# Kernel tuning notes

Measured on AMD Instinct MI355X. Metric: run time of the kernel, lower is better.

## Reference

```python
import jax, jax.numpy as jnp
import numpy as np

HIER_WEIGHT = 0.1

def setup_inputs() -> dict:
    key = jax.random.key(0)
    k1, k2, k3, k4, k5 = jax.random.split(key, 5)
    B, N, D = 128, 100000, 256
    E = N - 1
    return {
        "logits": jax.random.normal(k1, (B, N), dtype=jnp.float32),
        "labels": jax.random.randint(k2, (B,), 0, N, dtype=jnp.int64),
        "label_emb": jax.random.normal(k3, (N, D), dtype=jnp.float32),
        "parent_idx": jax.random.randint(k4, (E,), 0, N, dtype=jnp.int64),
        "child_idx": jax.random.randint(k5, (E,), 0, N, dtype=jnp.int64),
    }

def reference(logits, labels, label_emb, parent_idx, child_idx):
    # base loss: mean cross-entropy over the batch (loss_fn)
    logp = jax.nn.log_softmax(logits, axis=-1)                      # [B, N]
    ce = -jnp.take_along_axis(logp, labels[:, None], axis=-1)       # [B, 1]
    base_loss = jnp.mean(ce)
    # hierarchy penalty: sum over all (parent, child) edges of ||p - c||_2^2
    diff = label_emb[parent_idx] - label_emb[child_idx]             # [E, D]
    recursive_loss = jnp.sum(diff * diff)
    return base_loss + HIER_WEIGHT * recursive_loss
```

## Files before the change

### kernel.cpp

```cpp
#include <hip/hip_runtime.h>
#include <math.h>


#define CE_SLICES   8
#define CE_THREADS  256
#define EDGE_BATCH  32
#define EDGE_THREADS 256

__global__ __launch_bounds__(CE_THREADS) void ce_partial_kernel(
    const float* __restrict__ logits, float* __restrict__ ws_ce, int N)
{
    const int row   = blockIdx.x >> 3;
    const int slice = blockIdx.x & (CE_SLICES - 1);
    const int n4    = N >> 2;
    const int per   = n4 / CE_SLICES;
    const float4* __restrict__ rp4 =
        (const float4*)(logits + (size_t)row * (size_t)N) + (size_t)slice * per;
    const float L2E = 1.4426950408889634f;

    float s = 0.0f;
    for (int i = threadIdx.x; i < per; i += CE_THREADS) {
        float4 v = rp4[i];
        s += exp2f(v.x * L2E) + exp2f(v.y * L2E)
           + exp2f(v.z * L2E) + exp2f(v.w * L2E);
    }
    if (slice == CE_SLICES - 1) {
        const int rem = N & 3;
        if ((int)threadIdx.x < rem) {
            const float* rp = logits + (size_t)row * (size_t)N;
            s += exp2f(rp[(size_t)(n4 << 2) + threadIdx.x] * L2E);
        }
    }

    #pragma unroll
    for (int off = 32; off; off >>= 1) s += __shfl_xor(s, off);
    __shared__ float red[CE_THREADS / 64];
    const int lane = threadIdx.x & 63, wv = threadIdx.x >> 6;
    if (lane == 0) red[wv] = s;
    __syncthreads();
    if (threadIdx.x == 0) {
        float t = 0.0f;
        #pragma unroll
        for (int i = 0; i < CE_THREADS / 64; ++i) t += red[i];
        ws_ce[blockIdx.x] = t;
    }
}

__global__ __launch_bounds__(EDGE_THREADS) void edge_kernel(
    const float* __restrict__ emb, const int* __restrict__ parent,
    const int* __restrict__ child, float* __restrict__ ws_edge,
    int D, int E)
{
    const int lane = threadIdx.x & 63;
    const int wv   = threadIdx.x >> 6;
    const int wave = blockIdx.x * (EDGE_THREADS / 64) + wv;
    const int base = wave * EDGE_BATCH;
    const int d4   = D >> 2;

    float acc = 0.0f;
    if (base < E) {
        const int n = min(EDGE_BATCH, E - base);
        int idx = 0;
        if (lane < EDGE_BATCH) {
            if (lane < n) idx = parent[base + lane];
        } else {
            const int j = lane - EDGE_BATCH;
            if (j < n) idx = child[base + j];
        }
        const float4* __restrict__ emb4 = (const float4*)emb;

        if (d4 == 64) {
            #pragma unroll 4
            for (int j = 0; j < n; ++j) {
                const int p = __shfl(idx, j);
                const int c = __shfl(idx, j + EDGE_BATCH);
                float4 a = emb4[(size_t)p * 64 + lane];
                float4 b = emb4[(size_t)c * 64 + lane];
                float dx = a.x - b.x, dy = a.y - b.y;
                float dz = a.z - b.z, dw = a.w - b.w;
                acc += dx * dx + dy * dy + dz * dz + dw * dw;
            }
        } else {
            for (int j = 0; j < n; ++j) {
                const int p = __shfl(idx, j);
                const int c = __shfl(idx, j + EDGE_BATCH);
                for (int d = lane; d < d4; d += 64) {
                    float4 a = emb4[(size_t)p * d4 + d];
                    float4 b = emb4[(size_t)c * d4 + d];
                    float dx = a.x - b.x, dy = a.y - b.y;
                    float dz = a.z - b.z, dw = a.w - b.w;
                    acc += dx * dx + dy * dy + dz * dz + dw * dw;
                }
            }
        }
    }

    #pragma unroll
    for (int off = 32; off; off >>= 1) acc += __shfl_xor(acc, off);
    __shared__ float red[EDGE_THREADS / 64];
    if (lane == 0) red[wv] = acc;
    __syncthreads();
    if (threadIdx.x == 0) {
        float t = 0.0f;
        #pragma unroll
        for (int i = 0; i < EDGE_THREADS / 64; ++i) t += red[i];
        ws_edge[blockIdx.x] = t;
    }
}

__global__ __launch_bounds__(256) void finish_kernel(
    const float* __restrict__ logits, const int* __restrict__ labels,
    const float* __restrict__ ws_ce, const float* __restrict__ ws_edge,
    float* __restrict__ out, int B, int N, int n_edge_blocks)
{
    const int tid = threadIdx.x;
    float v = 0.0f;
    for (int r = tid; r < B; r += 256) {
        float s = 0.0f;
        #pragma unroll
        for (int k = 0; k < CE_SLICES; ++k) s += ws_ce[r * CE_SLICES + k];
        const int lab = labels[r];
        v += (logf(s) - logits[(size_t)r * (size_t)N + lab]) / (float)B;
    }
    float e = 0.0f;
    for (int i = tid; i < n_edge_blocks; i += 256) e += ws_edge[i];
    v += 0.1f * e;

    #pragma unroll
    for (int off = 32; off; off >>= 1) v += __shfl_xor(v, off);
    __shared__ float red[4];
    if ((tid & 63) == 0) red[tid >> 6] = v;
    __syncthreads();
    if (tid == 0) out[0] = red[0] + red[1] + red[2] + red[3];
}

extern "C" void kernel_launch(void* const* d_in, const int* in_sizes, int n_in,
                              void* d_out, int out_size, void* d_ws, size_t ws_size,
                              hipStream_t stream) {
    const float* logits = (const float*)d_in[0];
    const int*   labels = (const int*)d_in[1];
    const float* emb    = (const float*)d_in[2];
    const int*   parent = (const int*)d_in[3];
    const int*   child  = (const int*)d_in[4];
    float* out = (float*)d_out;

    const int B = in_sizes[1];
    const int N = in_sizes[0] / B;
    const int E = in_sizes[3];
    const int D = in_sizes[2] / N;

    const int n_waves       = (E + EDGE_BATCH - 1) / EDGE_BATCH;
    const int n_edge_blocks = (n_waves + (EDGE_THREADS/64) - 1) / (EDGE_THREADS/64);

    float* ws_ce   = (float*)d_ws;
    float* ws_edge = ws_ce + (size_t)B * CE_SLICES;

    hipLaunchKernelGGL(ce_partial_kernel, dim3(B * CE_SLICES), dim3(CE_THREADS),
                       0, stream, logits, ws_ce, N);
    hipLaunchKernelGGL(edge_kernel, dim3(n_edge_blocks), dim3(EDGE_THREADS),
                       0, stream, emb, parent, child, ws_edge, D, E);
    hipLaunchKernelGGL(finish_kernel, dim3(1), dim3(256), 0, stream,
                       logits, labels, ws_ce, ws_edge, out, B, N, n_edge_blocks);
}
```

Before: 46.88 us.

## Fuse CE and edge kernels into one persistent wave-level work-unit kernel

Merges the cross-entropy partial-sum kernel and the edge-gather kernel into one persistent kernel with a fixed grid of 2048 blocks. Each wave grabs independent work units: 16-edge batches or CE row slices. The edge path uses a software-pipelined unrolled gather that keeps four parent/child row loads in flight, and reads indices with scalar loads instead of shuffles. Block-level reductions are dropped in favour of per-wave partials, which removes a kernel launch and syncthreads. In exchange, finish_kernel must now sum about 6250 edge partials with only one block, and CE units run as single waves after all edge units.

```diff
diff --git a/kernel.cpp b/kernel.cpp
--- a/kernel.cpp
+++ b/kernel.cpp
@@ -2,116 +2,112 @@
 #include <math.h>
 
 
-#define CE_SLICES   8
-#define CE_THREADS  256
-#define EDGE_BATCH  32
-#define EDGE_THREADS 256
+#define TPB   256
+#define WPB   (TPB / 64)
+#define EB    16
+#define NBLK  2048
+#define CE_SLICES 8
 
-__global__ __launch_bounds__(CE_THREADS) void ce_partial_kernel(
-    const float* __restrict__ logits, float* __restrict__ ws_ce, int N)
-{
-    const int row   = blockIdx.x >> 3;
-    const int slice = blockIdx.x & (CE_SLICES - 1);
-    const int n4    = N >> 2;
-    const int per   = n4 / CE_SLICES;
-    const float4* __restrict__ rp4 =
-        (const float4*)(logits + (size_t)row * (size_t)N) + (size_t)slice * per;
-    const float L2E = 1.4426950408889634f;
-
-    float s = 0.0f;
-    for (int i = threadIdx.x; i < per; i += CE_THREADS) {
-        float4 v = rp4[i];
-        s += exp2f(v.x * L2E) + exp2f(v.y * L2E)
-           + exp2f(v.z * L2E) + exp2f(v.w * L2E);
-    }
-    if (slice == CE_SLICES - 1) {
-        const int rem = N & 3;
-        if ((int)threadIdx.x < rem) {
-            const float* rp = logits + (size_t)row * (size_t)N;
-            s += exp2f(rp[(size_t)(n4 << 2) + threadIdx.x] * L2E);
-        }
-    }
-
-    #pragma unroll
-    for (int off = 32; off; off >>= 1) s += __shfl_xor(s, off);
-    __shared__ float red[CE_THREADS / 64];
-    const int lane = threadIdx.x & 63, wv = threadIdx.x >> 6;
-    if (lane == 0) red[wv] = s;
-    __syncthreads();
-    if (threadIdx.x == 0) {
-        float t = 0.0f;
-        #pragma unroll
-        for (int i = 0; i < CE_THREADS / 64; ++i) t += red[i];
-        ws_ce[blockIdx.x] = t;
-    }
-}
-
-__global__ __launch_bounds__(EDGE_THREADS) void edge_kernel(
-    const float* __restrict__ emb, const int* __restrict__ parent,
-    const int* __restrict__ child, float* __restrict__ ws_edge,
-    int D, int E)
+__global__ __launch_bounds__(TPB, 8) void work_kernel(
+    const float* __restrict__ logits,
+    const float* __restrict__ emb,
+    const int* __restrict__ parent,
+    const int* __restrict__ child,
+    float* __restrict__ ws_edge,
+    float* __restrict__ ws_ce,
+    int N, int D, int E, int n_edge_units, int n_units)
 {
     const int lane = threadIdx.x & 63;
-    const int wv   = threadIdx.x >> 6;
-    const int wave = blockIdx.x * (EDGE_THREADS / 64) + wv;
-    const int base = wave * EDGE_BATCH;
-    const int d4   = D >> 2;
+    const int wvu  = __builtin_amdgcn_readfirstlane((int)(threadIdx.x >> 6));
+    const int wave = (int)blockIdx.x * WPB + wvu;
+    const int n_waves = (int)gridDim.x * WPB;
+    const int d4 = D >> 2;
+    const float L2E = 1.4426950408889634f;
+    const float4* __restrict__ emb4 = (const float4*)emb;
 
-    float acc = 0.0f;
-    if (base < E) {
-        const int n = min(EDGE_BATCH, E - base);
-        int idx = 0;
-        if (lane < EDGE_BATCH) {
-            if (lane < n) idx = parent[base + lane];
-        } else {
-            const int j = lane - EDGE_BATCH;
-            if (j < n) idx = child[base + j];
-        }
-        const float4* __restrict__ emb4 = (const float4*)emb;
+    for (int u = wave; u < n_units; u += n_waves) {
+        if (u < n_edge_units) {
+            const int base = u * EB;
+            const int n = min(EB, E - base);
+            float acc = 0.0f;
 
-        if (d4 == 64) {
-            #pragma unroll 4
-            for (int j = 0; j < n; ++j) {
-                const int p = __shfl(idx, j);
-                const int c = __shfl(idx, j + EDGE_BATCH);
-                float4 a = emb4[(size_t)p * 64 + lane];
-                float4 b = emb4[(size_t)c * 64 + lane];
-                float dx = a.x - b.x, dy = a.y - b.y;
-                float dz = a.z - b.z, dw = a.w - b.w;
-                acc += dx * dx + dy * dy + dz * dz + dw * dw;
-            }
-        } else {
-            for (int j = 0; j < n; ++j) {
-                const int p = __shfl(idx, j);
-                const int c = __shfl(idx, j + EDGE_BATCH);
-                for (int d = lane; d < d4; d += 64) {
-                    float4 a = emb4[(size_t)p * d4 + d];
-                    float4 b = emb4[(size_t)c * d4 + d];
-                    float dx = a.x - b.x, dy = a.y - b.y;
-                    float dz = a.z - b.z, dw = a.w - b.w;
-                    acc += dx * dx + dy * dy + dz * dz + dw * dw;
+            if (n == EB && d4 == 64) {
+                float4 a0, b0, a1, b1, a2, b2, a3, b3;
+#define EISSUE(K, J) { \
+    const int pp_ = parent[base + (J)]; \
+    const int cc_ = child[base + (J)]; \
+    a##K = emb4[(size_t)pp_ * 64 + lane]; \
+    b##K = emb4[(size_t)cc_ * 64 + lane]; }
+#define ECONS(K) { \
+    const float dx_ = a##K.x - b##K.x, dy_ = a##K.y - b##K.y; \
+    const float dz_ = a##K.z - b##K.z, dw_ = a##K.w - b##K.w; \
+    acc += dx_ * dx_ + dy_ * dy_ + dz_ * dz_ + dw_ * dw_; }
+                EISSUE(0, 0)  EISSUE(1, 1)  EISSUE(2, 2)  EISSUE(3, 3)
+                ECONS(0) EISSUE(0, 4)
+                ECONS(1) EISSUE(1, 5)
+                ECONS(2) EISSUE(2, 6)
+                ECONS(3) EISSUE(3, 7)
+                ECONS(0) EISSUE(0, 8)
+                ECONS(1) EISSUE(1, 9)
+                ECONS(2) EISSUE(2, 10)
+                ECONS(3) EISSUE(3, 11)
+                ECONS(0) EISSUE(0, 12)
+                ECONS(1) EISSUE(1, 13)
+                ECONS(2) EISSUE(2, 14)
+                ECONS(3) EISSUE(3, 15)
+                ECONS(0) ECONS(1) ECONS(2) ECONS(3)
+#undef EISSUE
+#undef ECONS
+            } else {
+                for (int j = 0; j < n; ++j) {
+                    const int pp = parent[base + j];
+                    const int cc = child[base + j];
+                    for (int d = lane; d < d4; d += 64) {
+                        float4 a = emb4[(size_t)pp * d4 + d];
+                        float4 b = emb4[(size_t)cc * d4 + d];
+                        const float dx = a.x - b.x, dy = a.y - b.y;
+                        const float dz = a.z - b.z, dw = a.w - b.w;
+                        acc += dx * dx + dy * dy + dz * dz + dw * dw;
+                    }
                 }
             }
+            #pragma unroll
+            for (int off = 32; off; off >>= 1) acc += __shfl_xor(acc, off);
+            if (lane == 0) ws_edge[u] = acc;
+        } else {
+            const int cu    = u - n_edge_units;
+            const int row   = cu >> 3;
+            const int slice = cu & (CE_SLICES - 1);
+            const int n4    = N >> 2;
+            const int per   = n4 / CE_SLICES;
+            const float4* __restrict__ rp4 =
+                (const float4*)(logits + (size_t)row * (size_t)N)
+                + (size_t)slice * per;
+
+            float s = 0.0f;
+            for (int i = lane; i < per; i += 64) {
+                float4 v = rp4[i];
+                s += exp2f(v.x * L2E) + exp2f(v.y * L2E)
+                   + exp2f(v.z * L2E) + exp2f(v.w * L2E);
+            }
+            if (slice == CE_SLICES - 1) {
+                const int rem = N & 3;
+                if (lane < rem) {
+                    const float* rp = logits + (size_t)row * (size_t)N;
+                    s += exp2f(rp[(size_t)(n4 << 2) + lane] * L2E);
+                }
+            }
+            #pragma unroll
+            for (int off = 32; off; off >>= 1) s += __shfl_xor(s, off);
+            if (lane == 0) ws_ce[cu] = s;
         }
-    }
-
-    #pragma unroll
-    for (int off = 32; off; off >>= 1) acc += __shfl_xor(acc, off);
-    __shared__ float red[EDGE_THREADS / 64];
-    if (lane == 0) red[wv] = acc;
-    __syncthreads();
-    if (threadIdx.x == 0) {
-        float t = 0.0f;
-        #pragma unroll
-        for (int i = 0; i < EDGE_THREADS / 64; ++i) t += red[i];
-        ws_edge[blockIdx.x] = t;
     }
 }
 
 __global__ __launch_bounds__(256) void finish_kernel(
     const float* __restrict__ logits, const int* __restrict__ labels,
     const float* __restrict__ ws_ce, const float* __restrict__ ws_edge,
-    float* __restrict__ out, int B, int N, int n_edge_blocks)
+    float* __restrict__ out, int B, int N, int n_edge_units)
 {
     const int tid = threadIdx.x;
     float v = 0.0f;
@@ -123,7 +119,7 @@
         v += (logf(s) - logits[(size_t)r * (size_t)N + lab]) / (float)B;
     }
     float e = 0.0f;
-    for (int i = tid; i < n_edge_blocks; i += 256) e += ws_edge[i];
+    for (int i = tid; i < n_edge_units; i += 256) e += ws_edge[i];
     v += 0.1f * e;
 
     #pragma unroll
@@ -149,16 +145,16 @@
     const int E = in_sizes[3];
     const int D = in_sizes[2] / N;
 
-    const int n_waves       = (E + EDGE_BATCH - 1) / EDGE_BATCH;
-    const int n_edge_blocks = (n_waves + (EDGE_THREADS/64) - 1) / (EDGE_THREADS/64);
+    const int n_edge_units = (E + EB - 1) / EB;
+    const int n_ce_units   = B * CE_SLICES;
+    const int n_units      = n_edge_units + n_ce_units;
 
-    float* ws_ce   = (float*)d_ws;
-    float* ws_edge = ws_ce + (size_t)B * CE_SLICES;
+    float* ws_edge = (float*)d_ws;
+    float* ws_ce   = ws_edge + n_edge_units;
 
-    hipLaunchKernelGGL(ce_partial_kernel, dim3(B * CE_SLICES), dim3(CE_THREADS),
-                       0, stream, logits, ws_ce, N);
-    hipLaunchKernelGGL(edge_kernel, dim3(n_edge_blocks), dim3(EDGE_THREADS),
-                       0, stream, emb, parent, child, ws_edge, D, E);
+    hipLaunchKernelGGL(work_kernel, dim3(NBLK), dim3(TPB), 0, stream,
+                       logits, emb, parent, child, ws_edge, ws_ce,
+                       N, D, E, n_edge_units, n_units);
     hipLaunchKernelGGL(finish_kernel, dim3(1), dim3(256), 0, stream,
-                       logits, labels, ws_ce, ws_edge, out, B, N, n_edge_blocks);
+                       logits, labels, ws_ce, ws_edge, out, B, N, n_edge_units);
 }
```

Result: slower. 59.77 us (+27.5%).
